# Kernel tuning notes

Hardware: AMD Instinct MI355X
Metric: run time of the kernel (lower is better)

## Reference

```python
import jax, jax.numpy as jnp
import numpy as np


def setup_inputs() -> dict:
    key = jax.random.key(0)
    k1, k2, k3, k4, k5 = jax.random.split(key, 5)
    B, S, DK, D = 64, 2048, 1024, 1024
    hidden_state = jax.random.normal(k1, (B, D), dtype=jnp.float32)
    encoder_outputs = jax.random.normal(k2, (B, S, DK), dtype=jnp.float32)
    # linear1: in = dim_key + dim*num_layers = 2048, out = dim = 1024
    W1 = jax.random.normal(k3, (D, DK + D), dtype=jnp.float32) * (1.0 / np.sqrt(DK + D))
    b1 = jax.random.normal(k4, (D,), dtype=jnp.float32) * 0.01
    W2 = jax.random.normal(k5, (1, D), dtype=jnp.float32) * (1.0 / np.sqrt(D))
    return {"hidden_state": hidden_state, "encoder_outputs": encoder_outputs,
            "W1": W1, "b1": b1, "W2": W2}


def reference(hidden_state, encoder_outputs, W1, b1, W2):
    # torch: cat([enc, h], -1) @ W1.T  ==  enc @ W1e.T + h @ W1h.T
    # (split avoids materializing the [B,S,DK+D] concat; same math)
    DK = encoder_outputs.shape[-1]
    W1e, W1h = W1[:, :DK], W1[:, DK:]
    # pre: [B, S, D]
    pre = (jnp.einsum('bsk,dk->bsd', encoder_outputs, W1e)
           + jnp.einsum('bm,dm->bd', hidden_state, W1h)[:, None, :]
           + b1)
    e = jnp.einsum('bsd,d->bs', jnp.tanh(pre), W2[0])  # scores [B, S]
    alpha = jax.nn.softmax(e, axis=1)
    context = jnp.einsum('bs,bsk->bk', alpha, encoder_outputs)  # [B, DK]
    return context
```

## Files before the change

### kernel.cpp

```cpp
#include <hip/hip_runtime.h>

typedef __attribute__((ext_vector_type(8))) short short8;
typedef __attribute__((ext_vector_type(4))) float floatx4;

#define M_TOT 131072
#define SEQ   2048
#define NB    8

__device__ __forceinline__ unsigned bf16rne(float x) {
  unsigned u = __float_as_uint(x);
  return (u + 0x7FFFu + ((u >> 16) & 1u)) >> 16;
}

__device__ __forceinline__ unsigned cvtpk_bf16(float lo, float hi) {
  unsigned r;
  asm("v_cvt_pk_bf16_f32 %0, %1, %2" : "=v"(r) : "v"(lo), "v"(hi));
  return r;
}

#define GLOAD_LDS16(g, l) __builtin_amdgcn_global_load_lds( \
    (const __attribute__((address_space(1))) unsigned int*)(g), \
    (__attribute__((address_space(3))) unsigned int*)(l), 16, 0, 0)

__global__ __launch_bounds__(128) void convert_w1e_frag_kernel(
    const float* __restrict__ W1, unsigned int* __restrict__ out)
{
  int d = blockIdx.x;
  int kc = threadIdx.x;
  const float* p = W1 + (size_t)d * 2048 + kc * 8;
  float4 a = *(const float4*)p;
  float4 b = *(const float4*)(p + 4);
  uint4 o;
  o.x = bf16rne(a.x) | (bf16rne(a.y) << 16);
  o.y = bf16rne(a.z) | (bf16rne(a.w) << 16);
  o.z = bf16rne(b.x) | (bf16rne(b.y) << 16);
  o.w = bf16rne(b.z) | (bf16rne(b.w) << 16);
  int nb = d >> 7, f = (d >> 4) & 7, t = kc >> 2;
  int lane = (d & 15) + ((kc & 3) << 4);
  size_t chunk = ((size_t)(nb * 32 + t) * 8 + f) * 64 + lane;
  *(uint4*)(out + chunk * 4) = o;
}

__global__ __launch_bounds__(256) void hvec_kernel(
    const float* __restrict__ hid, const float* __restrict__ W1,
    const float* __restrict__ b1, float* __restrict__ hvec)
{
  int b = blockIdx.x, g = blockIdx.y;
  int w = threadIdx.x >> 6, lane = threadIdx.x & 63;
  const float* hrow = hid + b * 1024;
  for (int i = 0; i < 4; ++i) {
    int d = g * 16 + w * 4 + i;
    const float* wrow = W1 + (size_t)d * 2048 + 1024;
    float sum = 0.f;
#pragma unroll
    for (int c = 0; c < 4; ++c) {
      int m = c * 256 + lane * 4;
      float4 wv = *(const float4*)(wrow + m);
      float4 hv = *(const float4*)(hrow + m);
      sum += wv.x * hv.x + wv.y * hv.y + wv.z * hv.z + wv.w * hv.w;
    }
#pragma unroll
    for (int msk = 1; msk < 64; msk <<= 1) sum += __shfl_xor(sum, msk);
    if (lane == 0) hvec[b * 1024 + d] = sum + b1[d];
  }
}

__global__ __launch_bounds__(256, 3) void gemm128_kernel(
    const float* __restrict__ enc, const unsigned short* __restrict__ Bfrag,
    const float* __restrict__ W2, const float* __restrict__ hvec,
    float* __restrict__ epart)
{
  __shared__ __align__(16) unsigned short ldsA[2][4096];
  __shared__ __align__(16) unsigned short ldsB[4][4096];

  const int tid = threadIdx.x;
  const int lid = blockIdx.x;
  const int xcd = lid & 7, q = lid >> 3;
  const int mb = xcd * 128 + (q >> 3);
  const int nb = q & 7;
  const int r0 = mb * 128;
  const int bidx = mb >> 4;
  const int wid = tid >> 6, lane = tid & 63;
  const int wm = wid >> 1, wn = wid & 1;
  const int lrow = lane & 15, kq = lane >> 4;

  const float* aSrc[2];
  int aDst[2];
#pragma unroll
  for (int j = 0; j < 2; ++j) {
    int c = tid + j * 256, row = c >> 2, kc = c & 3;
    aSrc[j] = enc + (size_t)(r0 + row) * 1024 + kc * 8;
    aDst[j] = ((row >> 4) * 64 + (row & 15) + (kc << 4)) * 8;
  }
  const unsigned short* bBase = Bfrag + (size_t)nb * 32 * 4096;

  floatx4 acc[4][4];
#pragma unroll
  for (int i = 0; i < 4; ++i)
#pragma unroll
    for (int j = 0; j < 4; ++j)
      acc[i][j] = (floatx4){0.f, 0.f, 0.f, 0.f};

  float4 aR[2][2];
#pragma unroll
  for (int j = 0; j < 2; ++j) {
    aR[j][0] = *(const float4*)(aSrc[j]);
    aR[j][1] = *(const float4*)(aSrc[j] + 4);
  }
  GLOAD_LDS16(bBase + tid * 8,         &ldsB[0][wid * 512]);
  GLOAD_LDS16(bBase + (tid + 256) * 8, &ldsB[0][wid * 512 + 2048]);

  const int aOff = wm * 2048 + lane * 8;
  const int bOff = wn * 2048 + lane * 8;

  for (int tt = 0; tt < 8; ++tt) {
#pragma unroll
    for (int u = 0; u < 4; ++u) {
      const int t = tt * 4 + u;
      const int sA = u & 1;
      const int sB = u;
      const int sBn = (u + 1) & 3;
#pragma unroll
      for (int j = 0; j < 2; ++j) {
        uint4 o;
        o.x = cvtpk_bf16(aR[j][0].x, aR[j][0].y);
        o.y = cvtpk_bf16(aR[j][0].z, aR[j][0].w);
        o.z = cvtpk_bf16(aR[j][1].x, aR[j][1].y);
        o.w = cvtpk_bf16(aR[j][1].z, aR[j][1].w);
        *(uint4*)&ldsA[sA][aDst[j]] = o;
      }
      const bool more = (u < 3) || (tt < 7);
      if (more) {
#pragma unroll
        for (int j = 0; j < 2; ++j) {
          aR[j][0] = *(const float4*)(aSrc[j] + (t + 1) * 32);
          aR[j][1] = *(const float4*)(aSrc[j] + (t + 1) * 32 + 4);
        }
        GLOAD_LDS16(bBase + (size_t)(t + 1) * 4096 + tid * 8,
                    &ldsB[sBn][wid * 512]);
        GLOAD_LDS16(bBase + (size_t)(t + 1) * 4096 + (tid + 256) * 8,
                    &ldsB[sBn][wid * 512 + 2048]);
        asm volatile("s_waitcnt vmcnt(6)" ::: "memory");
      } else {
        asm volatile("s_waitcnt vmcnt(0)" ::: "memory");
      }
      asm volatile("s_waitcnt lgkmcnt(0)" ::: "memory");
      __builtin_amdgcn_s_barrier();
      short8 af[4], bf[4];
#pragma unroll
      for (int mt = 0; mt < 4; ++mt)
        af[mt] = *(const short8*)&ldsA[sA][aOff + mt * 512];
#pragma unroll
      for (int nt = 0; nt < 4; ++nt)
        bf[nt] = *(const short8*)&ldsB[sB][bOff + nt * 512];
      __builtin_amdgcn_s_setprio(1);
#pragma unroll
      for (int mt = 0; mt < 4; ++mt)
#pragma unroll
        for (int nt = 0; nt < 4; ++nt)
          acc[mt][nt] = __builtin_amdgcn_mfma_f32_16x16x32_bf16(
              af[mt], bf[nt], acc[mt][nt], 0, 0, 0);
      __builtin_amdgcn_s_setprio(0);
    }
  }

  __syncthreads();
  float* ep = (float*)&ldsA[0][0];
  float hv[4], w2v[4];
#pragma unroll
  for (int nt = 0; nt < 4; ++nt) {
    int n = nb * 128 + wn * 64 + nt * 16 + lrow;
    hv[nt]  = hvec[bidx * 1024 + n];
    w2v[nt] = W2[n];
  }
#pragma unroll
  for (int mt = 0; mt < 4; ++mt) {
#pragma unroll
    for (int r = 0; r < 4; ++r) {
      float sum = 0.f;
#pragma unroll
      for (int nt = 0; nt < 4; ++nt) {
        float pre = acc[mt][nt][r] + hv[nt];
        float ex = __expf(2.f * pre);
        sum += (1.f - 2.f / (ex + 1.f)) * w2v[nt];
      }
      sum += __shfl_xor(sum, 1);
      sum += __shfl_xor(sum, 2);
      sum += __shfl_xor(sum, 4);
      sum += __shfl_xor(sum, 8);
      if (lrow == 0) ep[wn * 128 + wm * 64 + mt * 16 + kq * 4 + r] = sum;
    }
  }
  __syncthreads();
  if (tid < 128)
    epart[(size_t)nb * M_TOT + r0 + tid] = ep[tid] + ep[128 + tid];
}

__global__ __launch_bounds__(256) void fused_gemm_kernel(
    const float* __restrict__ enc, const float* __restrict__ W1,
    const float* __restrict__ W2, const float* __restrict__ hvec,
    float* __restrict__ epart)
{
  __shared__ __align__(16) unsigned short Ah[128 * 32];
  __shared__ __align__(16) unsigned short Bh[128 * 32];
  __shared__ float ep[2][128];

  const int tid = threadIdx.x;
  const int nb = blockIdx.x, mb = blockIdx.y;
  const int r0 = mb * 128, n0 = nb * 128;
  const int bidx = r0 >> 11;
  const int w = tid >> 6, lane = tid & 63;
  const int wm = w >> 1, wn = w & 1;
  const int lrow = lane & 15, kq = lane >> 4;

  floatx4 acc[4][4];
#pragma unroll
  for (int i = 0; i < 4; ++i)
#pragma unroll
    for (int j = 0; j < 4; ++j)
      acc[i][j] = (floatx4){0.f, 0.f, 0.f, 0.f};

  const int srow = tid >> 3;
  const int scol = (tid & 7) * 4;
  const float* aptr = enc + (size_t)(r0 + srow) * 1024 + scol;
  const float* bptr = W1  + (size_t)(n0 + srow) * 2048 + scol;

  for (int k0 = 0; k0 < 1024; k0 += 32) {
    float4 av[4], bv[4];
#pragma unroll
    for (int j = 0; j < 4; ++j) {
      av[j] = *(const float4*)(aptr + (size_t)(j * 32) * 1024 + k0);
      bv[j] = *(const float4*)(bptr + (size_t)(j * 32) * 2048 + k0);
    }
    __syncthreads();
#pragma unroll
    for (int j = 0; j < 4; ++j) {
      unsigned ax = __float_as_uint(av[j].x), ay = __float_as_uint(av[j].y);
      unsigned az = __float_as_uint(av[j].z), aw = __float_as_uint(av[j].w);
      unsigned a01 = __builtin_amdgcn_perm(ay, ax, 0x07060302u);
      unsigned a23 = __builtin_amdgcn_perm(aw, az, 0x07060302u);
      *(uint2*)&Ah[(tid + j * 256) * 4] = make_uint2(a01, a23);
      unsigned bx = __float_as_uint(bv[j].x), by = __float_as_uint(bv[j].y);
      unsigned bz = __float_as_uint(bv[j].z), bw = __float_as_uint(bv[j].w);
      unsigned b01 = __builtin_amdgcn_perm(by, bx, 0x07060302u);
      unsigned b23 = __builtin_amdgcn_perm(bw, bz, 0x07060302u);
      *(uint2*)&Bh[(tid + j * 256) * 4] = make_uint2(b01, b23);
    }
    __syncthreads();

    short8 af[4], bfm[4];
#pragma unroll
    for (int t4 = 0; t4 < 4; ++t4) {
      af[t4]  = *(const short8*)&Ah[(wm * 64 + t4 * 16 + lrow) * 32 + kq * 8];
      bfm[t4] = *(const short8*)&Bh[(wn * 64 + t4 * 16 + lrow) * 32 + kq * 8];
    }
#pragma unroll
    for (int mt = 0; mt < 4; ++mt)
#pragma unroll
      for (int nt = 0; nt < 4; ++nt)
        acc[mt][nt] = __builtin_amdgcn_mfma_f32_16x16x32_bf16(
            af[mt], bfm[nt], acc[mt][nt], 0, 0, 0);
  }

  float hv[4], w2v[4];
#pragma unroll
  for (int nt = 0; nt < 4; ++nt) {
    int n = n0 + wn * 64 + nt * 16 + lrow;
    hv[nt]  = hvec[bidx * 1024 + n];
    w2v[nt] = W2[n];
  }
#pragma unroll
  for (int mt = 0; mt < 4; ++mt) {
#pragma unroll
    for (int r = 0; r < 4; ++r) {
      float sum = 0.f;
#pragma unroll
      for (int nt = 0; nt < 4; ++nt) {
        float pre = acc[mt][nt][r] + hv[nt];
        float ex = __expf(2.f * pre);
        sum += (1.f - 2.f / (ex + 1.f)) * w2v[nt];
      }
      sum += __shfl_xor(sum, 1);
      sum += __shfl_xor(sum, 2);
      sum += __shfl_xor(sum, 4);
      sum += __shfl_xor(sum, 8);
      if (lrow == 0) ep[wn][wm * 64 + mt * 16 + kq * 4 + r] = sum;
    }
  }
  __syncthreads();
  if (tid < 128)
    epart[(size_t)nb * M_TOT + r0 + tid] = ep[0][tid] + ep[1][tid];
}

__global__ __launch_bounds__(256) void softmax_kernel(
    const float* __restrict__ epart, float* __restrict__ alpha)
{
  int b = blockIdx.x, t = threadIdx.x;
  __shared__ float redmax[4], redsum[4];
  float ev[8];
  float lmax = -1e30f;
#pragma unroll
  for (int j = 0; j < 8; ++j) {
    int s = t + j * 256;
    float sum = 0.f;
#pragma unroll
    for (int p = 0; p < 8; ++p) sum += epart[(size_t)p * M_TOT + b * SEQ + s];
    ev[j] = sum;
    lmax = fmaxf(lmax, sum);
  }
#pragma unroll
  for (int msk = 1; msk < 64; msk <<= 1) lmax = fmaxf(lmax, __shfl_xor(lmax, msk));
  if ((t & 63) == 0) redmax[t >> 6] = lmax;
  __syncthreads();
  float bmax = fmaxf(fmaxf(redmax[0], redmax[1]), fmaxf(redmax[2], redmax[3]));
  float lsum = 0.f;
#pragma unroll
  for (int j = 0; j < 8; ++j) { ev[j] = __expf(ev[j] - bmax); lsum += ev[j]; }
#pragma unroll
  for (int msk = 1; msk < 64; msk <<= 1) lsum += __shfl_xor(lsum, msk);
  if ((t & 63) == 0) redsum[t >> 6] = lsum;
  __syncthreads();
  float inv = 1.f / (redsum[0] + redsum[1] + redsum[2] + redsum[3]);
#pragma unroll
  for (int j = 0; j < 8; ++j) alpha[b * SEQ + t + j * 256] = ev[j] * inv;
}

__global__ __launch_bounds__(512) void context_f32_kernel(
    const float* __restrict__ enc, const float* __restrict__ alpha,
    float* __restrict__ out)
{
  __shared__ float red[16][128];
  int b = blockIdx.x, kc = blockIdx.y, t = threadIdx.x;
  int kl = (t & 31) * 4;
  int strip = t >> 5;
  const float* ep = enc + ((size_t)b * SEQ + strip * 128) * 1024 + kc * 128 + kl;
  const float* ap = alpha + b * SEQ + strip * 128;
  float a0 = 0.f, a1 = 0.f, a2 = 0.f, a3 = 0.f;
#pragma unroll 4
  for (int s = 0; s < 128; ++s) {
    float a = ap[s];
    float4 v = *(const float4*)(ep + (size_t)s * 1024);
    a0 += a * v.x; a1 += a * v.y; a2 += a * v.z; a3 += a * v.w;
  }
  red[strip][kl + 0] = a0;
  red[strip][kl + 1] = a1;
  red[strip][kl + 2] = a2;
  red[strip][kl + 3] = a3;
  __syncthreads();
  if (t < 128) {
    float s = 0.f;
#pragma unroll
    for (int j = 0; j < 16; ++j) s += red[j][t];
    out[b * 1024 + kc * 128 + t] = s;
  }
}

__global__ __launch_bounds__(256) void context_kernel(
    const float* __restrict__ enc, const float* __restrict__ alpha,
    float* __restrict__ out)
{
  int b = blockIdx.y, sq = blockIdx.z, t = threadIdx.x;
  int k4 = t * 4;
  const float* ep = enc + ((size_t)b * SEQ + sq * 128) * 1024 + k4;
  const float* ap = alpha + b * SEQ + sq * 128;
  float ax = 0.f, ay = 0.f, az = 0.f, aw = 0.f;
#pragma unroll 4
  for (int s = 0; s < 128; ++s) {
    float a = ap[s];
    float4 v = *(const float4*)(ep + (size_t)s * 1024);
    ax += a * v.x; ay += a * v.y; az += a * v.z; aw += a * v.w;
  }
  float* o = out + b * 1024 + k4;
  atomicAdd(o + 0, ax);
  atomicAdd(o + 1, ay);
  atomicAdd(o + 2, az);
  atomicAdd(o + 3, aw);
}

extern "C" void kernel_launch(void* const* d_in, const int* in_sizes, int n_in,
                              void* d_out, int out_size, void* d_ws, size_t ws_size,
                              hipStream_t stream) {
  const float* hid = (const float*)d_in[0];
  const float* enc = (const float*)d_in[1];
  const float* W1  = (const float*)d_in[2];
  const float* b1  = (const float*)d_in[3];
  const float* W2  = (const float*)d_in[4];
  float* out = (float*)d_out;

  float* epart = (float*)d_ws;
  float* alpha = epart + (size_t)NB * M_TOT;
  float* hvec  = alpha + M_TOT;
  size_t small_bytes = ((size_t)NB * M_TOT + M_TOT + 64 * 1024) * 4;
  size_t w1eb_off = ((small_bytes + 255) / 256) * 256;
  size_t need = w1eb_off + (size_t)1024 * 1024 * 2;

  hvec_kernel<<<dim3(64, 64), 256, 0, stream>>>(hid, W1, b1, hvec);

  if (ws_size >= need) {
    unsigned short* W1eB = (unsigned short*)((char*)d_ws + w1eb_off);
    convert_w1e_frag_kernel<<<1024, 128, 0, stream>>>(W1, (unsigned int*)W1eB);
    gemm128_kernel<<<8192, 256, 0, stream>>>(enc, W1eB, W2, hvec, epart);
    softmax_kernel<<<64, 256, 0, stream>>>(epart, alpha);
    context_f32_kernel<<<dim3(64, 8), 512, 0, stream>>>(enc, alpha, out);
  } else {
    hipMemsetAsync(d_out, 0, (size_t)out_size * sizeof(float), stream);
    fused_gemm_kernel<<<dim3(NB, 1024), 256, 0, stream>>>(enc, W1, W2, hvec, epart);
    softmax_kernel<<<64, 256, 0, stream>>>(epart, alpha);
    context_kernel<<<dim3(1, 64, 16), 256, 0, stream>>>(enc, alpha, out);
  }
}
```

Measured before the change: 1.130 ms.

## Pre-convert encoder to bf16 fragment layout and use 256x128 GEMM tiles

Adds a separate pass that converts the fp32 encoder outputs into a bf16 MFMA-fragment layout in workspace, so the GEMM streams both operands straight into LDS with global_load_lds instead of loading fp32 into registers and converting. The GEMM tile grows to 256x128 with 512 threads and triple-buffered LDS, which halves how many times W1e is re-read per row. The cost is an extra full read of the 512MB encoder plus a 256MB bf16 write and a re-read, a larger workspace requirement, and more launches. If the workspace is too small the slower fallback path runs.

```diff
diff --git a/kernel.cpp b/kernel.cpp
--- a/kernel.cpp
+++ b/kernel.cpp
@@ -12,22 +12,19 @@
   return (u + 0x7FFFu + ((u >> 16) & 1u)) >> 16;
 }
 
-__device__ __forceinline__ unsigned cvtpk_bf16(float lo, float hi) {
-  unsigned r;
-  asm("v_cvt_pk_bf16_f32 %0, %1, %2" : "=v"(r) : "v"(lo), "v"(hi));
-  return r;
-}
-
 #define GLOAD_LDS16(g, l) __builtin_amdgcn_global_load_lds( \
     (const __attribute__((address_space(1))) unsigned int*)(g), \
     (__attribute__((address_space(3))) unsigned int*)(l), 16, 0, 0)
 
-__global__ __launch_bounds__(128) void convert_w1e_frag_kernel(
-    const float* __restrict__ W1, unsigned int* __restrict__ out)
-{
-  int d = blockIdx.x;
-  int kc = threadIdx.x;
-  const float* p = W1 + (size_t)d * 2048 + kc * 8;
+__global__ __launch_bounds__(256) void convert_enc_frag_kernel(
+    const float* __restrict__ in, unsigned int* __restrict__ out)
+{
+  unsigned C = blockIdx.x * 256 + threadIdx.x;
+  int l = C & 63, mt = (C >> 6) & 3, wm = (C >> 8) & 3;
+  int t = (C >> 10) & 31, mb = C >> 15;
+  int row = mb * 256 + wm * 64 + mt * 16 + (l & 15);
+  int k0  = t * 32 + (l >> 4) * 8;
+  const float* p = in + (size_t)row * 1024 + k0;
   float4 a = *(const float4*)p;
   float4 b = *(const float4*)(p + 4);
   uint4 o;
@@ -35,10 +32,26 @@
   o.y = bf16rne(a.z) | (bf16rne(a.w) << 16);
   o.z = bf16rne(b.x) | (bf16rne(b.y) << 16);
   o.w = bf16rne(b.z) | (bf16rne(b.w) << 16);
-  int nb = d >> 7, f = (d >> 4) & 7, t = kc >> 2;
-  int lane = (d & 15) + ((kc & 3) << 4);
-  size_t chunk = ((size_t)(nb * 32 + t) * 8 + f) * 64 + lane;
-  *(uint4*)(out + chunk * 4) = o;
+  *(uint4*)(out + (size_t)C * 4) = o;
+}
+
+__global__ __launch_bounds__(256) void convert_w1e_frag_kernel(
+    const float* __restrict__ W1, unsigned int* __restrict__ out)
+{
+  unsigned G = blockIdx.x * 256 + threadIdx.x;
+  int l = G & 63, nt = (G >> 6) & 3, wn = (G >> 8) & 1;
+  int t = (G >> 9) & 31, nb = G >> 14;
+  int d  = nb * 128 + wn * 64 + nt * 16 + (l & 15);
+  int k0 = t * 32 + (l >> 4) * 8;
+  const float* p = W1 + (size_t)d * 2048 + k0;
+  float4 a = *(const float4*)p;
+  float4 b = *(const float4*)(p + 4);
+  uint4 o;
+  o.x = bf16rne(a.x) | (bf16rne(a.y) << 16);
+  o.y = bf16rne(a.z) | (bf16rne(a.w) << 16);
+  o.z = bf16rne(b.x) | (bf16rne(b.y) << 16);
+  o.w = bf16rne(b.z) | (bf16rne(b.w) << 16);
+  *(uint4*)(out + (size_t)G * 4) = o;
 }
 
 __global__ __launch_bounds__(256) void hvec_kernel(
@@ -65,34 +78,25 @@
   }
 }
 
-__global__ __launch_bounds__(256, 3) void gemm128_kernel(
-    const float* __restrict__ enc, const unsigned short* __restrict__ Bfrag,
+__global__ __launch_bounds__(512, 4) void gemm256x128_kernel(
+    const unsigned short* __restrict__ encB, const unsigned short* __restrict__ W1eB,
     const float* __restrict__ W2, const float* __restrict__ hvec,
     float* __restrict__ epart)
 {
-  __shared__ __align__(16) unsigned short ldsA[2][4096];
-  __shared__ __align__(16) unsigned short ldsB[4][4096];
+  __shared__ __align__(16) unsigned short ldsA[3][8192];
+  __shared__ __align__(16) unsigned short ldsB[3][4096];
 
   const int tid = threadIdx.x;
   const int lid = blockIdx.x;
   const int xcd = lid & 7, q = lid >> 3;
-  const int mb = xcd * 128 + (q >> 3);
+  const int mb = xcd * 64 + (q >> 3);
   const int nb = q & 7;
-  const int r0 = mb * 128;
-  const int bidx = mb >> 4;
+  const int r0 = mb * 256;
+  const int bidx = mb >> 3;
   const int wid = tid >> 6, lane = tid & 63;
   const int wm = wid >> 1, wn = wid & 1;
   const int lrow = lane & 15, kq = lane >> 4;
-
-  const float* aSrc[2];
-  int aDst[2];
-#pragma unroll
-  for (int j = 0; j < 2; ++j) {
-    int c = tid + j * 256, row = c >> 2, kc = c & 3;
-    aSrc[j] = enc + (size_t)(r0 + row) * 1024 + kc * 8;
-    aDst[j] = ((row >> 4) * 64 + (row & 15) + (kc << 4)) * 8;
-  }
-  const unsigned short* bBase = Bfrag + (size_t)nb * 32 * 4096;
+  const int lane8 = lane * 8;
 
   floatx4 acc[4][4];
 #pragma unroll
@@ -101,67 +105,49 @@
     for (int j = 0; j < 4; ++j)
       acc[i][j] = (floatx4){0.f, 0.f, 0.f, 0.f};
 
-  float4 aR[2][2];
-#pragma unroll
-  for (int j = 0; j < 2; ++j) {
-    aR[j][0] = *(const float4*)(aSrc[j]);
-    aR[j][1] = *(const float4*)(aSrc[j] + 4);
-  }
-  GLOAD_LDS16(bBase + tid * 8,         &ldsB[0][wid * 512]);
-  GLOAD_LDS16(bBase + (tid + 256) * 8, &ldsB[0][wid * 512 + 2048]);
-
-  const int aOff = wm * 2048 + lane * 8;
-  const int bOff = wn * 2048 + lane * 8;
-
-  for (int tt = 0; tt < 8; ++tt) {
-#pragma unroll
-    for (int u = 0; u < 4; ++u) {
-      const int t = tt * 4 + u;
-      const int sA = u & 1;
-      const int sB = u;
-      const int sBn = (u + 1) & 3;
-#pragma unroll
-      for (int j = 0; j < 2; ++j) {
-        uint4 o;
-        o.x = cvtpk_bf16(aR[j][0].x, aR[j][0].y);
-        o.y = cvtpk_bf16(aR[j][0].z, aR[j][0].w);
-        o.z = cvtpk_bf16(aR[j][1].x, aR[j][1].y);
-        o.w = cvtpk_bf16(aR[j][1].z, aR[j][1].w);
-        *(uint4*)&ldsA[sA][aDst[j]] = o;
-      }
-      const bool more = (u < 3) || (tt < 7);
-      if (more) {
-#pragma unroll
-        for (int j = 0; j < 2; ++j) {
-          aR[j][0] = *(const float4*)(aSrc[j] + (t + 1) * 32);
-          aR[j][1] = *(const float4*)(aSrc[j] + (t + 1) * 32 + 4);
-        }
-        GLOAD_LDS16(bBase + (size_t)(t + 1) * 4096 + tid * 8,
-                    &ldsB[sBn][wid * 512]);
-        GLOAD_LDS16(bBase + (size_t)(t + 1) * 4096 + (tid + 256) * 8,
-                    &ldsB[sBn][wid * 512 + 2048]);
-        asm volatile("s_waitcnt vmcnt(6)" ::: "memory");
-      } else {
-        asm volatile("s_waitcnt vmcnt(0)" ::: "memory");
-      }
-      asm volatile("s_waitcnt lgkmcnt(0)" ::: "memory");
-      __builtin_amdgcn_s_barrier();
-      short8 af[4], bf[4];
-#pragma unroll
-      for (int mt = 0; mt < 4; ++mt)
-        af[mt] = *(const short8*)&ldsA[sA][aOff + mt * 512];
+  unsigned short *aCur = ldsA[0], *aNx = ldsA[1], *aN2 = ldsA[2];
+  unsigned short *bCur = ldsB[0], *bNx = ldsB[1], *bN2 = ldsB[2];
+
+  {
+    const unsigned short* ga = encB + ((size_t)mb * 32 * 1024 + tid) * 8;
+    GLOAD_LDS16(ga,        &aCur[wid * 512]);
+    GLOAD_LDS16(ga + 4096, &aCur[4096 + wid * 512]);
+    const unsigned short* gb = W1eB + ((size_t)nb * 32 * 512 + tid) * 8;
+    GLOAD_LDS16(gb,        &bCur[wid * 512]);
+  }
+
+  const int aRd = wm * 2048 + lane8;
+  const int bRd = wn * 2048 + lane8;
+
+  for (int t = 0; t < 32; ++t) {
+    if (t < 31) {
+      const unsigned short* ga = encB + ((size_t)(mb * 32 + t + 1) * 1024 + tid) * 8;
+      GLOAD_LDS16(ga,        &aNx[wid * 512]);
+      GLOAD_LDS16(ga + 4096, &aNx[4096 + wid * 512]);
+      const unsigned short* gb = W1eB + ((size_t)(nb * 32 + t + 1) * 512 + tid) * 8;
+      GLOAD_LDS16(gb,        &bNx[wid * 512]);
+      asm volatile("s_waitcnt vmcnt(3)" ::: "memory");
+    } else {
+      asm volatile("s_waitcnt vmcnt(0)" ::: "memory");
+    }
+    __builtin_amdgcn_s_barrier();
+
+    short8 af[4], bf[4];
+#pragma unroll
+    for (int mt = 0; mt < 4; ++mt) af[mt] = *(const short8*)&aCur[aRd + mt * 512];
+#pragma unroll
+    for (int nt = 0; nt < 4; ++nt) bf[nt] = *(const short8*)&bCur[bRd + nt * 512];
+    __builtin_amdgcn_s_setprio(1);
+#pragma unroll
+    for (int mt = 0; mt < 4; ++mt)
 #pragma unroll
       for (int nt = 0; nt < 4; ++nt)
-        bf[nt] = *(const short8*)&ldsB[sB][bOff + nt * 512];
-      __builtin_amdgcn_s_setprio(1);
-#pragma unroll
-      for (int mt = 0; mt < 4; ++mt)
-#pragma unroll
-        for (int nt = 0; nt < 4; ++nt)
-          acc[mt][nt] = __builtin_amdgcn_mfma_f32_16x16x32_bf16(
-              af[mt], bf[nt], acc[mt][nt], 0, 0, 0);
-      __builtin_amdgcn_s_setprio(0);
-    }
+        acc[mt][nt] = __builtin_amdgcn_mfma_f32_16x16x32_bf16(
+            af[mt], bf[nt], acc[mt][nt], 0, 0, 0);
+    __builtin_amdgcn_s_setprio(0);
+
+    unsigned short* tA = aCur; aCur = aNx; aNx = aN2; aN2 = tA;
+    unsigned short* tB = bCur; bCur = bNx; bNx = bN2; bN2 = tB;
   }
 
   __syncthreads();
@@ -188,12 +174,12 @@
       sum += __shfl_xor(sum, 2);
       sum += __shfl_xor(sum, 4);
       sum += __shfl_xor(sum, 8);
-      if (lrow == 0) ep[wn * 128 + wm * 64 + mt * 16 + kq * 4 + r] = sum;
-    }
-  }
-  __syncthreads();
-  if (tid < 128)
-    epart[(size_t)nb * M_TOT + r0 + tid] = ep[tid] + ep[128 + tid];
+      if (lrow == 0) ep[wn * 256 + wm * 64 + mt * 16 + kq * 4 + r] = sum;
+    }
+  }
+  __syncthreads();
+  if (tid < 256)
+    epart[(size_t)nb * M_TOT + r0 + tid] = ep[tid] + ep[256 + tid];
 }
 
 __global__ __launch_bounds__(256) void fused_gemm_kernel(
@@ -391,15 +377,17 @@
   float* alpha = epart + (size_t)NB * M_TOT;
   float* hvec  = alpha + M_TOT;
   size_t small_bytes = ((size_t)NB * M_TOT + M_TOT + 64 * 1024) * 4;
-  size_t w1eb_off = ((small_bytes + 255) / 256) * 256;
-  size_t need = w1eb_off + (size_t)1024 * 1024 * 2;
+  size_t encB_off = ((small_bytes + 255) / 256) * 256;
+  size_t need = encB_off + (size_t)M_TOT * 1024 * 2 + (size_t)1024 * 1024 * 2;
 
   hvec_kernel<<<dim3(64, 64), 256, 0, stream>>>(hid, W1, b1, hvec);
 
   if (ws_size >= need) {
-    unsigned short* W1eB = (unsigned short*)((char*)d_ws + w1eb_off);
-    convert_w1e_frag_kernel<<<1024, 128, 0, stream>>>(W1, (unsigned int*)W1eB);
-    gemm128_kernel<<<8192, 256, 0, stream>>>(enc, W1eB, W2, hvec, epart);
+    unsigned short* encB = (unsigned short*)((char*)d_ws + encB_off);
+    unsigned short* W1eB = encB + (size_t)M_TOT * 1024;
+    convert_enc_frag_kernel<<<65536, 256, 0, stream>>>(enc, (unsigned int*)encB);
+    convert_w1e_frag_kernel<<<512, 256, 0, stream>>>(W1, (unsigned int*)W1eB);
+    gemm256x128_kernel<<<4096, 512, 0, stream>>>(encB, W1eB, W2, hvec, epart);
     softmax_kernel<<<64, 256, 0, stream>>>(epart, alpha);
     context_f32_kernel<<<dim3(64, 8), 512, 0, stream>>>(enc, alpha, out);
   } else {
```

Result: no change. 1.137 ms (+0.6%).
